# Performance work log

Measured on AMD Instinct MI355X. Metric: run time of the kernel, lower is better.

## Reference

```python
import jax, jax.numpy as jnp
import numpy as np

DIM = 1024
NUM_HEADS = 16
HEAD_DIM = DIM // NUM_HEADS


def setup_inputs() -> dict:
    key = jax.random.key(0)
    k1, k2, k3, k4 = jax.random.split(key, 4)
    x = jax.random.normal(k1, (4, 4096, DIM), dtype=jnp.float32)
    # nn.Linear(dim, 3*dim, bias=False): weight [3*dim, dim]
    w_qkv = jax.random.normal(k2, (3 * DIM, DIM), dtype=jnp.float32) * (1.0 / np.sqrt(DIM))
    # nn.Linear(dim, dim): weight [dim, dim], bias [dim]
    w_proj = jax.random.normal(k3, (DIM, DIM), dtype=jnp.float32) * (1.0 / np.sqrt(DIM))
    b_proj = jax.random.normal(k4, (DIM,), dtype=jnp.float32) * 0.01
    return {"x": x, "w_qkv": w_qkv, "w_proj": w_proj, "b_proj": b_proj}


def reference(x, w_qkv, w_proj, b_proj):
    B, N, C = x.shape
    H, D = NUM_HEADS, C // NUM_HEADS
    # qkv projection: [B,N,3C] -> [3,B,H,N,D]
    qkv = (x @ w_qkv.T).reshape(B, N, 3, H, D).transpose(2, 0, 3, 1, 4)
    q, k, v = qkv[0], qkv[1], qkv[2]
    # elu(x)+1 feature map
    q = jax.nn.elu(q) + 1.0
    k = jax.nn.elu(k) + 1.0
    # kv outer-product aggregation: [B,H,D,D]
    kv = jnp.einsum('bhnd,bhne->bhde', k, v)
    # numerator: [B,H,N,D]
    num = jnp.einsum('bhnd,bhde->bhne', q, kv)
    # normalizer: [B,H,N]
    z = 1.0 / (jnp.einsum('bhnd,bhd->bhn', q, k.sum(axis=2)) + 1e-6)
    out = num * z[..., None]  # [B,H,N,D]
    out = out.transpose(0, 2, 1, 3).reshape(B, N, C)
    return out @ w_proj.T + b_proj
```

## Files before the change

### kernel.cpp

```cpp
#include <hip/hip_runtime.h>
#include <hip/hip_bf16.h>
#include <stdint.h>


typedef unsigned short u16;
typedef __attribute__((ext_vector_type(4))) float f32x4;
typedef __attribute__((ext_vector_type(8))) __bf16 bf16x8;
typedef __attribute__((ext_vector_type(4))) unsigned short us4;
typedef __attribute__((ext_vector_type(8))) unsigned short us8;

typedef __attribute__((address_space(3))) unsigned as3u;
typedef const __attribute__((address_space(1))) unsigned as1u;

__device__ __forceinline__ float bf2f(u16 u) {
  union { unsigned i; float f; } x; x.i = ((unsigned)u) << 16; return x.f;
}
__device__ __forceinline__ u16 f2bf(float f) {
  union { float f; unsigned i; } x; x.f = f;
  return (u16)((x.i + 0x7FFFu + ((x.i >> 16) & 1u)) >> 16);
}
__device__ __forceinline__ void gload16(const u16* g, u16* l) {
  __builtin_amdgcn_global_load_lds((as1u*)g, (as3u*)l, 16, 0, 0);
}
__device__ __forceinline__ bf16x8 ld8(const u16* p) { return *(const bf16x8*)p; }

#define BAR asm volatile("s_barrier" ::: "memory")
#define VMC4 asm volatile("s_waitcnt vmcnt(4)" ::: "memory")
#define VMC0 asm volatile("s_waitcnt vmcnt(0)" ::: "memory")

__global__ __launch_bounds__(256) void cvt_kernel(const float* __restrict__ src,
                                                  u16* __restrict__ dst, int n4) {
  int i = blockIdx.x * 256 + threadIdx.x;
  if (i < n4) {
    f32x4 v = ((const f32x4*)src)[i];
    us4 o;
    o[0] = f2bf(v[0]); o[1] = f2bf(v[1]); o[2] = f2bf(v[2]); o[3] = f2bf(v[3]);
    ((us4*)dst)[i] = o;
  }
}

template <int EPI>
__global__ __launch_bounds__(512) void gemm256(
    const u16* __restrict__ A, const u16* __restrict__ B, int Ncols,
    u16* __restrict__ oQ, u16* __restrict__ oKT, u16* __restrict__ oVT,
    const float* __restrict__ bias, float* __restrict__ oF) {
  constexpr int K = 1024;
  constexpr int NITER = 8;
  __shared__ u16 lds[2][2][256 * 64];

  const int bid = blockIdx.x;
  const int tm = (bid & 7) * 8 + ((bid >> 3) & 7);
  const int tn = bid >> 6;
  const int m0 = tm << 8, n0 = tn << 8;
  const int t = threadIdx.x;
  const int w = t >> 6, lane = t & 63;
  const int wm = w >> 2, wn = w & 3;
  const int l15 = lane & 15, l4 = lane >> 4;

  const u16* Ab = A + (size_t)m0 * K;
  const u16* Bb = B + (size_t)n0 * K;

  int srcoff[2][2];
  #pragma unroll
  for (int l = 0; l < 2; ++l) {
    int c = l * 512 + t;
    int row = c >> 3, ch = c & 7;
    #pragma unroll
    for (int h = 0; h < 2; ++h) {
      int r = row + h * 128;
      srcoff[l][h] = r * K + (ch ^ (r & 7)) * 8;
    }
  }

#define STAGE(mat, buf, h, kt)                                                \
  {                                                                           \
    const u16* gsrc = ((mat) ? Bb : Ab) + (kt) * 64;                          \
    _Pragma("unroll") for (int l = 0; l < 2; ++l)                             \
        gload16(gsrc + srcoff[l][h],                                          \
                &lds[buf][mat][(l * 512 + w * 64) * 8 + (h) * 128 * 64]);     \
  }

#define LDA(buf, q)                                                           \
  _Pragma("unroll") for (int i = 0; i < 2; ++i)                               \
  _Pragma("unroll") for (int kk = 0; kk < 2; ++kk) {                          \
    int row = wm * 128 + (q) * 32 + i * 16 + l15;                             \
    int ch = (kk * 4 + l4) ^ (row & 7);                                       \
    a[i][kk] = ld8(&lds[buf][0][row * 64 + ch * 8]);                          \
  }

#define LDB(buf)                                                              \
  _Pragma("unroll") for (int j = 0; j < 4; ++j)                               \
  _Pragma("unroll") for (int kk = 0; kk < 2; ++kk) {                          \
    int row = wn * 64 + j * 16 + l15;                                         \
    int ch = (kk * 4 + l4) ^ (row & 7);                                       \
    b[j][kk] = ld8(&lds[buf][1][row * 64 + ch * 8]);                          \
  }

#define MFMA16(q)                                                             \
  __builtin_amdgcn_s_setprio(1);                                              \
  _Pragma("unroll") for (int i = 0; i < 2; ++i)                               \
  _Pragma("unroll") for (int kk = 0; kk < 2; ++kk)                            \
  _Pragma("unroll") for (int j = 0; j < 4; ++j)                               \
    acc[(q) * 2 + i][j] = __builtin_amdgcn_mfma_f32_16x16x32_bf16(            \
        a[i][kk], b[j][kk], acc[(q) * 2 + i][j], 0, 0, 0);                    \
  __builtin_amdgcn_s_setprio(0);

  f32x4 acc[8][4] = {};
  bf16x8 a[2][2], b[4][2];

  STAGE(1, 0, 0, 0); STAGE(1, 0, 1, 0);
  STAGE(0, 0, 0, 0); STAGE(0, 0, 1, 0);
  STAGE(1, 1, 0, 1); STAGE(1, 1, 1, 1);
  VMC4;
  BAR;

  for (int J = 0; J < NITER; ++J) {
    const int t2 = 2 * J + 2, t3 = 2 * J + 3;
    const bool more = (J < NITER - 1);
    LDB(0); LDA(0, 0);
    STAGE(0, 1, 0, 2 * J + 1);
    BAR; MFMA16(0); BAR;
    LDA(0, 1);
    STAGE(0, 1, 1, 2 * J + 1);
    BAR; MFMA16(1); BAR;
    LDA(0, 2);
    if (more) STAGE(1, 0, 0, t2);
    BAR; MFMA16(2); BAR;
    LDA(0, 3);
    if (more) STAGE(1, 0, 1, t2);
    BAR; MFMA16(3);
    if (more) { VMC4; } else { VMC0; }
    BAR;
    LDB(1); LDA(1, 0);
    if (more) STAGE(0, 0, 0, t2);
    BAR; MFMA16(0); BAR;
    LDA(1, 1);
    if (more) STAGE(0, 0, 1, t2);
    BAR; MFMA16(1); BAR;
    LDA(1, 2);
    if (more) STAGE(1, 1, 0, t3);
    BAR; MFMA16(2); BAR;
    LDA(1, 3);
    if (more) STAGE(1, 1, 1, t3);
    BAR; MFMA16(3);
    if (more) { VMC4; } else { VMC0; }
    BAR;
  }

  if constexpr (EPI == 0) {
    const int part = n0 >> 10;
    if (part == 0) {
      u16* sb = (u16*)lds;
      __syncthreads();
      #pragma unroll
      for (int fi = 0; fi < 8; ++fi) {
        #pragma unroll
        for (int j = 0; j < 4; ++j) {
          #pragma unroll
          for (int r = 0; r < 4; ++r) {
            int m = wm * 128 + fi * 16 + l4 * 4 + r;
            int c = wn * 64 + j * 16 + l15;
            float val = acc[fi][j][r];
            val = val > 0.f ? val + 1.f : __expf(val);
            sb[m * 256 + (c ^ (((m >> 2) & 3) << 4))] = f2bf(val);
          }
        }
      }
      __syncthreads();
      #pragma unroll
      for (int i = 0; i < 16; ++i) {
        int idx = i * 512 + t;
        int rr = idx >> 5, g = idx & 31;
        int gs = g ^ (((rr >> 2) & 3) << 1);
        us8 vv = *(const us8*)&sb[rr * 256 + gs * 8];
        int n = (m0 + rr) & 4095, bb = (m0 + rr) >> 12;
        int c = n0 + g * 8;
        int h = c >> 6, d = c & 63;
        *(us8*)&oQ[(((size_t)(bb * 16 + h)) * 4096 + n) * 64 + d] = vv;
      }
    } else {
      #pragma unroll
      for (int j = 0; j < 4; ++j) {
        const int col = n0 + wn * 64 + j * 16 + l15;
        const int cc = col & 1023;
        const int h = cc >> 6, d = cc & 63;
        #pragma unroll
        for (int fi = 0; fi < 8; ++fi) {
          const int mbase = m0 + wm * 128 + fi * 16 + l4 * 4;
          const int bb = mbase >> 12, n = mbase & 4095;
          const int bh = bb * 16 + h;
          us4 o;
          #pragma unroll
          for (int r = 0; r < 4; ++r) {
            float val = acc[fi][j][r];
            if (part == 1) val = val > 0.f ? val + 1.f : __expf(val);
            o[r] = f2bf(val);
          }
          u16* dst = (part == 1) ? oKT : oVT;
          *(us4*)&dst[(((size_t)bh) * 64 + d) * 4096 + n] = o;
        }
      }
    }
  } else {
    #pragma unroll
    for (int fi = 0; fi < 8; ++fi) {
      const int mbase = m0 + wm * 128 + fi * 16 + l4 * 4;
      #pragma unroll
      for (int j = 0; j < 4; ++j) {
        const int col = n0 + wn * 64 + j * 16 + l15;
        #pragma unroll
        for (int r = 0; r < 4; ++r)
          oF[(size_t)(mbase + r) * 1024 + col] = acc[fi][j][r] + bias[col];
      }
    }
  }
#undef STAGE
#undef LDA
#undef LDB
#undef MFMA16
}

__global__ __launch_bounds__(256) void kv_mfma(const u16* __restrict__ kTg,
                                               const u16* __restrict__ vTg,
                                               float* __restrict__ kv_part,
                                               float* __restrict__ ksum_part) {
  __shared__ u16 kTl[64 * 256];
  __shared__ u16 vTl[64 * 256];
  const int blk = blockIdx.x;
  const int bh = blk >> 4, s = blk & 15;
  const int n0 = s * 256;
  const int t = threadIdx.x;
  const int w = t >> 6, lane = t & 63;
  const int wr = w >> 1, wc = w & 1;
  const int l15 = lane & 15, l4 = lane >> 4;

  const u16* kg = kTg + ((size_t)bh * 64) * 4096 + n0;
  const u16* vg = vTg + ((size_t)bh * 64) * 4096 + n0;
  #pragma unroll
  for (int i = 0; i < 8; ++i) {
    int c = i * 256 + t;
    int row = c >> 5, ch = c & 31;
    int sch = (ch & ~7) | ((ch ^ row) & 7);
    gload16(kg + (size_t)row * 4096 + sch * 8, &kTl[(i * 256 + w * 64) * 8]);
    gload16(vg + (size_t)row * 4096 + sch * 8, &vTl[(i * 256 + w * 64) * 8]);
  }
  __syncthreads();

  {
    const int row = t >> 2, q4 = t & 3;
    float sum = 0.f;
    #pragma unroll
    for (int j = 0; j < 8; ++j) {
      int p = q4 * 8 + ((j + row) & 7);
      us8 u = *(const us8*)&kTl[row * 256 + p * 8];
      #pragma unroll
      for (int x = 0; x < 8; ++x) sum += bf2f(u[x]);
    }
    sum += __shfl_xor(sum, 1);
    sum += __shfl_xor(sum, 2);
    if ((t & 3) == 0) ksum_part[((size_t)s * 64 + bh) * 64 + row] = sum;
  }

  f32x4 acc[2][2] = {};
  #pragma unroll
  for (int kk = 0; kk < 8; ++kk) {
    bf16x8 a[2], b[2];
    #pragma unroll
    for (int i = 0; i < 2; ++i) {
      int row = wr * 32 + i * 16 + l15;
      int p = (kk * 4 + l4) ^ (row & 7);
      a[i] = ld8(&kTl[row * 256 + p * 8]);
    }
    #pragma unroll
    for (int j = 0; j < 2; ++j) {
      int row = wc * 32 + j * 16 + l15;
      int p = (kk * 4 + l4) ^ (row & 7);
      b[j] = ld8(&vTl[row * 256 + p * 8]);
    }
    #pragma unroll
    for (int i = 0; i < 2; ++i)
      #pragma unroll
      for (int j = 0; j < 2; ++j)
        acc[i][j] = __builtin_amdgcn_mfma_f32_16x16x32_bf16(a[i], b[j], acc[i][j], 0, 0, 0);
  }
  float* dst = kv_part + ((size_t)s * 64 + bh) * 4096;
  #pragma unroll
  for (int i = 0; i < 2; ++i)
    #pragma unroll
    for (int j = 0; j < 2; ++j)
      #pragma unroll
      for (int r = 0; r < 4; ++r) {
        int d = wr * 32 + i * 16 + l4 * 4 + r;
        int e = wc * 32 + j * 16 + l15;
        dst[e * 64 + d] = acc[i][j][r];
      }
}

__global__ __launch_bounds__(256) void cvt_kv(const float* __restrict__ kv_part,
                                              const float* __restrict__ ksum_part,
                                              u16* __restrict__ kvTb) {
  const int bh = blockIdx.x;
  const int t = threadIdx.x;
  #pragma unroll
  for (int i = 0; i < 20; ++i) {
    int idx = i * 256 + t;
    int row = idx >> 6, d = idx & 63;
    float s = 0.f;
    if (row < 64) {
      #pragma unroll
      for (int p = 0; p < 16; ++p)
        s += kv_part[((size_t)p * 64 + bh) * 4096 + idx];
    } else if (row == 64) {
      #pragma unroll
      for (int p = 0; p < 16; ++p)
        s += ksum_part[((size_t)p * 64 + bh) * 64 + d];
    }
    kvTb[(size_t)bh * 5120 + idx] = f2bf(s);
  }
}

__global__ __launch_bounds__(256) void numz_mfma(const u16* __restrict__ qg,
                                                 const u16* __restrict__ kvTb,
                                                 u16* __restrict__ attn) {
  __shared__ u16 ql[128 * 64];
  __shared__ u16 bl[80 * 64];
  const int blk = blockIdx.x;
  const int bh = blk >> 5, c5 = blk & 31;
  const int t = threadIdx.x;
  const int w = t >> 6, lane = t & 63;
  const int l15 = lane & 15, l4 = lane >> 4;
  const int bb = bh >> 4, h = bh & 15;

  const u16* qp = qg + ((size_t)bh * 4096 + c5 * 128) * 64;
  #pragma unroll
  for (int i = 0; i < 4; ++i) {
    int c = i * 256 + t;
    int row = c >> 3, ch = c & 7;
    gload16(qp + (size_t)row * 64 + ((ch ^ row) & 7) * 8, &ql[(i * 256 + w * 64) * 8]);
  }
  {
    const us4* bsrc = (const us4*)(kvTb + (size_t)bh * 5120);
    #pragma unroll
    for (int i = 0; i < 5; ++i) {
      int idx = i * 256 + t;
      int row = idx >> 4;
      ((us4*)bl)[idx ^ ((row & 7) << 1)] = bsrc[idx];
    }
  }
  __syncthreads();

  f32x4 acc[2][5] = {};
  #pragma unroll
  for (int kk = 0; kk < 2; ++kk) {
    bf16x8 a[2], b[5];
    #pragma unroll
    for (int i = 0; i < 2; ++i) {
      int row = w * 32 + i * 16 + l15;
      int p = (kk * 4 + l4) ^ (row & 7);
      a[i] = ld8(&ql[row * 64 + p * 8]);
    }
    #pragma unroll
    for (int j = 0; j < 5; ++j) {
      int row = j * 16 + l15;
      int p = (kk * 4 + l4) ^ (row & 7);
      b[j] = ld8(&bl[row * 64 + p * 8]);
    }
    #pragma unroll
    for (int i = 0; i < 2; ++i)
      #pragma unroll
      for (int j = 0; j < 5; ++j)
        acc[i][j] = __builtin_amdgcn_mfma_f32_16x16x32_bf16(a[i], b[j], acc[i][j], 0, 0, 0);
  }

  #pragma unroll
  for (int i = 0; i < 2; ++i)
    #pragma unroll
    for (int r = 0; r < 4; ++r) {
      int m = w * 32 + i * 16 + l4 * 4 + r;
      int n = c5 * 128 + m;
      float zv = __shfl(acc[i][4][r], lane & 48);
      float zz = 1.f / (zv + 1e-6f);
      u16* op = attn + ((size_t)bb * 4096 + n) * 1024 + h * 64;
      #pragma unroll
      for (int j = 0; j < 4; ++j)
        op[j * 16 + l15] = f2bf(acc[i][j][r] * zz);
    }
}

extern "C" void kernel_launch(void* const* d_in, const int* in_sizes, int n_in,
                              void* d_out, int out_size, void* d_ws, size_t ws_size,
                              hipStream_t stream) {
  const float* x = (const float*)d_in[0];
  const float* w_qkv = (const float*)d_in[1];
  const float* w_proj = (const float*)d_in[2];
  const float* b_proj = (const float*)d_in[3];
  float* out = (float*)d_out;
  char* ws = (char*)d_ws;

  u16* xb        = (u16*)(ws);
  float* kv_part = (float*)(ws);
  u16* attn      = (u16*)(ws);
  u16* wqkvb     = (u16*)(ws + 33554432);
  u16* wprojb    = (u16*)(ws + 39845888);
  u16* q         = (u16*)(ws + 41943040);
  u16* kT        = (u16*)(ws + 75497472);
  u16* vT        = (u16*)(ws + 109051904);
  float* ksum_p  = (float*)(ws + 142606336);
  u16* kvTb      = (u16*)(ws + 142868480);

  cvt_kernel<<<16384, 256, 0, stream>>>(x, xb, 4194304);
  cvt_kernel<<<3072, 256, 0, stream>>>(w_qkv, wqkvb, 786432);
  cvt_kernel<<<1024, 256, 0, stream>>>(w_proj, wprojb, 262144);
  gemm256<0><<<64 * 12, 512, 0, stream>>>(xb, wqkvb, 3072, q, kT, vT, nullptr, nullptr);
  kv_mfma<<<1024, 256, 0, stream>>>(kT, vT, kv_part, ksum_p);
  cvt_kv<<<64, 256, 0, stream>>>(kv_part, ksum_p, kvTb);
  numz_mfma<<<2048, 256, 0, stream>>>(q, kvTb, attn);
  gemm256<1><<<64 * 4, 512, 0, stream>>>(attn, wprojb, 1024, nullptr, nullptr, nullptr,
                                         b_proj, out);
}
```

Baseline: 309.5 us.

## Fuse conversion launches, reduce kv via atomics, and remap GEMM tiles per XCD

Merges the three fp32-to-bf16 conversion kernels into one launch that also zeroes the kv and ksum accumulators. kv_mfma now processes 512 tokens per block and accumulates straight into the final kv/ksum buffers with float atomics, which removes the partial buffers and the separate cvt_kv reduction kernel. numz_mfma converts the fp32 kv to bf16 while loading it. The GEMM block-to-tile mapping is changed so that tiles sharing A rows stay on the same XCD. Atomics add contention and make the summation order nondeterministic.

Measured after the change: 329.1 us. 6.4% more time.

```diff
diff --git a/kernel.cpp b/kernel.cpp
--- a/kernel.cpp
+++ b/kernel.cpp
@@ -28,15 +28,26 @@
 #define VMC4 asm volatile("s_waitcnt vmcnt(4)" ::: "memory")
 #define VMC0 asm volatile("s_waitcnt vmcnt(0)" ::: "memory")
 
-__global__ __launch_bounds__(256) void cvt_kernel(const float* __restrict__ src,
-                                                  u16* __restrict__ dst, int n4) {
+#define CVT_O1 4194304
+#define CVT_O2 4980736
+#define CVT_O3 5242880
+#define CVT_O4 5309440
+__global__ __launch_bounds__(256) void cvt_all(
+    const float* __restrict__ x, const float* __restrict__ wqkv,
+    const float* __restrict__ wproj, u16* __restrict__ xb,
+    u16* __restrict__ wqkvb, u16* __restrict__ wprojb, float* __restrict__ kvz) {
   int i = blockIdx.x * 256 + threadIdx.x;
-  if (i < n4) {
-    f32x4 v = ((const f32x4*)src)[i];
-    us4 o;
-    o[0] = f2bf(v[0]); o[1] = f2bf(v[1]); o[2] = f2bf(v[2]); o[3] = f2bf(v[3]);
-    ((us4*)dst)[i] = o;
-  }
+  const float* src;
+  u16* dst;
+  int off;
+  if (i < CVT_O1) { src = x; dst = xb; off = i; }
+  else if (i < CVT_O2) { src = wqkv; dst = wqkvb; off = i - CVT_O1; }
+  else if (i < CVT_O3) { src = wproj; dst = wprojb; off = i - CVT_O2; }
+  else { ((f32x4*)kvz)[i - CVT_O3] = (f32x4){0.f, 0.f, 0.f, 0.f}; return; }
+  f32x4 v = ((const f32x4*)src)[off];
+  us4 o;
+  o[0] = f2bf(v[0]); o[1] = f2bf(v[1]); o[2] = f2bf(v[2]); o[3] = f2bf(v[3]);
+  ((us4*)dst)[off] = o;
 }
 
 template <int EPI>
@@ -48,9 +59,14 @@
   constexpr int NITER = 8;
   __shared__ u16 lds[2][2][256 * 64];
 
+  const int nTn = Ncols >> 8;
   const int bid = blockIdx.x;
-  const int tm = (bid & 7) * 8 + ((bid >> 3) & 7);
-  const int tn = bid >> 6;
+  const int xcd = bid & 7;
+  int r0 = bid >> 3;
+  const int p = r0 & 3; r0 >>= 2;
+  const int tn = r0 % nTn;
+  const int s = r0 / nTn;
+  const int tm = xcd * 8 + s * 4 + p;
   const int m0 = tm << 8, n0 = tn << 8;
   const int t = threadIdx.x;
   const int w = t >> 6, lane = t & 63;
@@ -67,8 +83,8 @@
     int row = c >> 3, ch = c & 7;
     #pragma unroll
     for (int h = 0; h < 2; ++h) {
-      int r = row + h * 128;
-      srcoff[l][h] = r * K + (ch ^ (r & 7)) * 8;
+      int rr = row + h * 128;
+      srcoff[l][h] = rr * K + (ch ^ (rr & 7)) * 8;
     }
   }
 
@@ -157,10 +173,10 @@
         #pragma unroll
         for (int j = 0; j < 4; ++j) {
           #pragma unroll
-          for (int r = 0; r < 4; ++r) {
-            int m = wm * 128 + fi * 16 + l4 * 4 + r;
+          for (int rr = 0; rr < 4; ++rr) {
+            int m = wm * 128 + fi * 16 + l4 * 4 + rr;
             int c = wn * 64 + j * 16 + l15;
-            float val = acc[fi][j][r];
+            float val = acc[fi][j][rr];
             val = val > 0.f ? val + 1.f : __expf(val);
             sb[m * 256 + (c ^ (((m >> 2) & 3) << 4))] = f2bf(val);
           }
@@ -191,10 +207,10 @@
           const int bh = bb * 16 + h;
           us4 o;
           #pragma unroll
-          for (int r = 0; r < 4; ++r) {
-            float val = acc[fi][j][r];
+          for (int rr = 0; rr < 4; ++rr) {
+            float val = acc[fi][j][rr];
             if (part == 1) val = val > 0.f ? val + 1.f : __expf(val);
-            o[r] = f2bf(val);
+            o[rr] = f2bf(val);
           }
           u16* dst = (part == 1) ? oKT : oVT;
           *(us4*)&dst[(((size_t)bh) * 64 + d) * 4096 + n] = o;
@@ -209,8 +225,8 @@
       for (int j = 0; j < 4; ++j) {
         const int col = n0 + wn * 64 + j * 16 + l15;
         #pragma unroll
-        for (int r = 0; r < 4; ++r)
-          oF[(size_t)(mbase + r) * 1024 + col] = acc[fi][j][r] + bias[col];
+        for (int rr = 0; rr < 4; ++rr)
+          oF[(size_t)(mbase + rr) * 1024 + col] = acc[fi][j][rr] + bias[col];
       }
     }
   }
@@ -222,105 +238,83 @@
 
 __global__ __launch_bounds__(256) void kv_mfma(const u16* __restrict__ kTg,
                                                const u16* __restrict__ vTg,
-                                               float* __restrict__ kv_part,
-                                               float* __restrict__ ksum_part) {
+                                               float* __restrict__ kv,
+                                               float* __restrict__ ksum) {
   __shared__ u16 kTl[64 * 256];
   __shared__ u16 vTl[64 * 256];
   const int blk = blockIdx.x;
-  const int bh = blk >> 4, s = blk & 15;
-  const int n0 = s * 256;
+  const int bh = blk >> 3, s = blk & 7;
   const int t = threadIdx.x;
   const int w = t >> 6, lane = t & 63;
   const int wr = w >> 1, wc = w & 1;
   const int l15 = lane & 15, l4 = lane >> 4;
-
-  const u16* kg = kTg + ((size_t)bh * 64) * 4096 + n0;
-  const u16* vg = vTg + ((size_t)bh * 64) * 4096 + n0;
-  #pragma unroll
-  for (int i = 0; i < 8; ++i) {
-    int c = i * 256 + t;
-    int row = c >> 5, ch = c & 31;
-    int sch = (ch & ~7) | ((ch ^ row) & 7);
-    gload16(kg + (size_t)row * 4096 + sch * 8, &kTl[(i * 256 + w * 64) * 8]);
-    gload16(vg + (size_t)row * 4096 + sch * 8, &vTl[(i * 256 + w * 64) * 8]);
-  }
-  __syncthreads();
-
-  {
-    const int row = t >> 2, q4 = t & 3;
-    float sum = 0.f;
+  const int srow = t >> 2, q4 = t & 3;
+
+  const u16* kg = kTg + ((size_t)bh * 64) * 4096 + s * 512;
+  const u16* vg = vTg + ((size_t)bh * 64) * 4096 + s * 512;
+
+  f32x4 acc[2][2] = {};
+  float sum = 0.f;
+  #pragma unroll
+  for (int it = 0; it < 2; ++it) {
+    __syncthreads();
+    #pragma unroll
+    for (int i = 0; i < 8; ++i) {
+      int c = i * 256 + t;
+      int row = c >> 5, ch = c & 31;
+      int sch = (ch & ~7) | ((ch ^ row) & 7);
+      gload16(kg + it * 256 + (size_t)row * 4096 + sch * 8, &kTl[(i * 256 + w * 64) * 8]);
+      gload16(vg + it * 256 + (size_t)row * 4096 + sch * 8, &vTl[(i * 256 + w * 64) * 8]);
+    }
+    __syncthreads();
     #pragma unroll
     for (int j = 0; j < 8; ++j) {
-      int p = q4 * 8 + ((j + row) & 7);
-      us8 u = *(const us8*)&kTl[row * 256 + p * 8];
-      #pragma unroll
-      for (int x = 0; x < 8; ++x) sum += bf2f(u[x]);
-    }
-    sum += __shfl_xor(sum, 1);
-    sum += __shfl_xor(sum, 2);
-    if ((t & 3) == 0) ksum_part[((size_t)s * 64 + bh) * 64 + row] = sum;
-  }
-
-  f32x4 acc[2][2] = {};
-  #pragma unroll
-  for (int kk = 0; kk < 8; ++kk) {
-    bf16x8 a[2], b[2];
-    #pragma unroll
-    for (int i = 0; i < 2; ++i) {
-      int row = wr * 32 + i * 16 + l15;
-      int p = (kk * 4 + l4) ^ (row & 7);
-      a[i] = ld8(&kTl[row * 256 + p * 8]);
-    }
-    #pragma unroll
-    for (int j = 0; j < 2; ++j) {
-      int row = wc * 32 + j * 16 + l15;
-      int p = (kk * 4 + l4) ^ (row & 7);
-      b[j] = ld8(&vTl[row * 256 + p * 8]);
-    }
-    #pragma unroll
-    for (int i = 0; i < 2; ++i)
-      #pragma unroll
-      for (int j = 0; j < 2; ++j)
-        acc[i][j] = __builtin_amdgcn_mfma_f32_16x16x32_bf16(a[i], b[j], acc[i][j], 0, 0, 0);
-  }
-  float* dst = kv_part + ((size_t)s * 64 + bh) * 4096;
+      int pp = q4 * 8 + ((j + srow) & 7);
+      us8 u = *(const us8*)&kTl[srow * 256 + pp * 8];
+      #pragma unroll
+      for (int x2 = 0; x2 < 8; ++x2) sum += bf2f(u[x2]);
+    }
+    #pragma unroll
+    for (int kk = 0; kk < 8; ++kk) {
+      bf16x8 a[2], b[2];
+      #pragma unroll
+      for (int i = 0; i < 2; ++i) {
+        int row = wr * 32 + i * 16 + l15;
+        int pp = (kk * 4 + l4) ^ (row & 7);
+        a[i] = ld8(&kTl[row * 256 + pp * 8]);
+      }
+      #pragma unroll
+      for (int j = 0; j < 2; ++j) {
+        int row = wc * 32 + j * 16 + l15;
+        int pp = (kk * 4 + l4) ^ (row & 7);
+        b[j] = ld8(&vTl[row * 256 + pp * 8]);
+      }
+      #pragma unroll
+      for (int i = 0; i < 2; ++i)
+        #pragma unroll
+        for (int j = 0; j < 2; ++j)
+          acc[i][j] = __builtin_amdgcn_mfma_f32_16x16x32_bf16(a[i], b[j], acc[i][j], 0, 0, 0);
+    }
+  }
+  sum += __shfl_xor(sum, 1);
+  sum += __shfl_xor(sum, 2);
+  if (q4 == 0) atomicAdd(&ksum[bh * 64 + srow], sum);
+  float* dst = kv + (size_t)bh * 4096;
   #pragma unroll
   for (int i = 0; i < 2; ++i)
     #pragma unroll
     for (int j = 0; j < 2; ++j)
       #pragma unroll
-      for (int r = 0; r < 4; ++r) {
-        int d = wr * 32 + i * 16 + l4 * 4 + r;
+      for (int rr = 0; rr < 4; ++rr) {
+        int d = wr * 32 + i * 16 + l4 * 4 + rr;
         int e = wc * 32 + j * 16 + l15;
-        dst[e * 64 + d] = acc[i][j][r];
-      }
-}
-
-__global__ __launch_bounds__(256) void cvt_kv(const float* __restrict__ kv_part,
-                                              const float* __restrict__ ksum_part,
-                                              u16* __restrict__ kvTb) {
-  const int bh = blockIdx.x;
-  const int t = threadIdx.x;
-  #pragma unroll
-  for (int i = 0; i < 20; ++i) {
-    int idx = i * 256 + t;
-    int row = idx >> 6, d = idx & 63;
-    float s = 0.f;
-    if (row < 64) {
-      #pragma unroll
-      for (int p = 0; p < 16; ++p)
-        s += kv_part[((size_t)p * 64 + bh) * 4096 + idx];
-    } else if (row == 64) {
-      #pragma unroll
-      for (int p = 0; p < 16; ++p)
-        s += ksum_part[((size_t)p * 64 + bh) * 64 + d];
-    }
-    kvTb[(size_t)bh * 5120 + idx] = f2bf(s);
-  }
+        atomicAdd(&dst[e * 64 + d], acc[i][j][rr]);
+      }
 }
 
 __global__ __launch_bounds__(256) void numz_mfma(const u16* __restrict__ qg,
-                                                 const u16* __restrict__ kvTb,
+                                                 const float* __restrict__ kv,
+                                                 const float* __restrict__ ksum,
                                                  u16* __restrict__ attn) {
   __shared__ u16 ql[128 * 64];
   __shared__ u16 bl[80 * 64];
@@ -339,12 +333,18 @@
     gload16(qp + (size_t)row * 64 + ((ch ^ row) & 7) * 8, &ql[(i * 256 + w * 64) * 8]);
   }
   {
-    const us4* bsrc = (const us4*)(kvTb + (size_t)bh * 5120);
+    const f32x4* kvp = (const f32x4*)(kv + (size_t)bh * 4096);
+    const f32x4* ksp = (const f32x4*)(ksum + bh * 64);
     #pragma unroll
     for (int i = 0; i < 5; ++i) {
       int idx = i * 256 + t;
-      int row = idx >> 4;
-      ((us4*)bl)[idx ^ ((row & 7) << 1)] = bsrc[idx];
+      int row = idx >> 4, u4 = idx & 15;
+      f32x4 v = {0.f, 0.f, 0.f, 0.f};
+      if (row < 64) v = kvp[idx];
+      else if (row == 64) v = ksp[u4];
+      us4 o;
+      o[0] = f2bf(v[0]); o[1] = f2bf(v[1]); o[2] = f2bf(v[2]); o[3] = f2bf(v[3]);
+      ((us4*)bl)[idx ^ ((row & 7) << 1)] = o;
     }
   }
   __syncthreads();
@@ -356,14 +356,14 @@
     #pragma unroll
     for (int i = 0; i < 2; ++i) {
       int row = w * 32 + i * 16 + l15;
-      int p = (kk * 4 + l4) ^ (row & 7);
-      a[i] = ld8(&ql[row * 64 + p * 8]);
+      int pp = (kk * 4 + l4) ^ (row & 7);
+      a[i] = ld8(&ql[row * 64 + pp * 8]);
     }
     #pragma unroll
     for (int j = 0; j < 5; ++j) {
       int row = j * 16 + l15;
-      int p = (kk * 4 + l4) ^ (row & 7);
-      b[j] = ld8(&bl[row * 64 + p * 8]);
+      int pp = (kk * 4 + l4) ^ (row & 7);
+      b[j] = ld8(&bl[row * 64 + pp * 8]);
     }
     #pragma unroll
     for (int i = 0; i < 2; ++i)
@@ -375,15 +375,15 @@
   #pragma unroll
   for (int i = 0; i < 2; ++i)
     #pragma unroll
-    for (int r = 0; r < 4; ++r) {
-      int m = w * 32 + i * 16 + l4 * 4 + r;
+    for (int rr = 0; rr < 4; ++rr) {
+      int m = w * 32 + i * 16 + l4 * 4 + rr;
       int n = c5 * 128 + m;
-      float zv = __shfl(acc[i][4][r], lane & 48);
+      float zv = __shfl(acc[i][4][rr], lane & 48);
       float zz = 1.f / (zv + 1e-6f);
       u16* op = attn + ((size_t)bb * 4096 + n) * 1024 + h * 64;
       #pragma unroll
       for (int j = 0; j < 4; ++j)
-        op[j * 16 + l15] = f2bf(acc[i][j][r] * zz);
+        op[j * 16 + l15] = f2bf(acc[i][j][rr] * zz);
     }
 }
 
@@ -398,23 +398,19 @@
   char* ws = (char*)d_ws;
 
   u16* xb        = (u16*)(ws);
-  float* kv_part = (float*)(ws);
   u16* attn      = (u16*)(ws);
   u16* wqkvb     = (u16*)(ws + 33554432);
   u16* wprojb    = (u16*)(ws + 39845888);
   u16* q         = (u16*)(ws + 41943040);
   u16* kT        = (u16*)(ws + 75497472);
   u16* vT        = (u16*)(ws + 109051904);
-  float* ksum_p  = (float*)(ws + 142606336);
-  u16* kvTb      = (u16*)(ws + 142868480);
-
-  cvt_kernel<<<16384, 256, 0, stream>>>(x, xb, 4194304);
-  cvt_kernel<<<3072, 256, 0, stream>>>(w_qkv, wqkvb, 786432);
-  cvt_kernel<<<1024, 256, 0, stream>>>(w_proj, wprojb, 262144);
+  float* kv      = (float*)(ws + 142606336);
+  float* ksum    = (float*)(ws + 143654912);
+
+  cvt_all<<<20740, 256, 0, stream>>>(x, w_qkv, w_proj, xb, wqkvb, wprojb, kv);
   gemm256<0><<<64 * 12, 512, 0, stream>>>(xb, wqkvb, 3072, q, kT, vT, nullptr, nullptr);
-  kv_mfma<<<1024, 256, 0, stream>>>(kT, vT, kv_part, ksum_p);
-  cvt_kv<<<64, 256, 0, stream>>>(kv_part, ksum_p, kvTb);
-  numz_mfma<<<2048, 256, 0, stream>>>(q, kvTb, attn);
+  kv_mfma<<<512, 256, 0, stream>>>(kT, vT, kv, ksum);
+  numz_mfma<<<2048, 256, 0, stream>>>(q, kv, ksum, attn);
   gemm256<1><<<64 * 4, 512, 0, stream>>>(attn, wprojb, 1024, nullptr, nullptr, nullptr,
                                          b_proj, out);
 }
```
